# Kernel optimization log

Measured on AMD Instinct MI355X. Metric: run time of the kernel, lower is better.

## Reference

```python
import jax, jax.numpy as jnp
import numpy as np

D_MODEL = 1024
N_HEADS = 16
D_K = D_MODEL // N_HEADS
D_FF = 4096
B, S = 4, 2048
EPS = 1e-5


def layer_norm(x, gamma, beta):
    mu = jnp.mean(x, axis=-1, keepdims=True)
    var = jnp.var(x, axis=-1, keepdims=True)
    return (x - mu) * jax.lax.rsqrt(var + EPS) * gamma + beta


def setup_inputs() -> dict:
    key = jax.random.key(0)
    ks = jax.random.split(key, 16)
    s = 1.0 / np.sqrt(D_MODEL)
    inp = {
        "query": jax.random.normal(ks[0], (B, S, D_MODEL), jnp.float32),
        "key": jax.random.normal(ks[1], (B, S, D_MODEL), jnp.float32),
        "value": jax.random.normal(ks[2], (B, S, D_MODEL), jnp.float32),
        "mask": jnp.ones((B, S, S), jnp.int32),
        "Wq": jax.random.normal(ks[3], (D_MODEL, D_MODEL), jnp.float32) * s,
        "Wk": jax.random.normal(ks[4], (D_MODEL, D_MODEL), jnp.float32) * s,
        "Wv": jax.random.normal(ks[5], (D_MODEL, D_MODEL), jnp.float32) * s,
        "Wo": jax.random.normal(ks[6], (D_MODEL, D_MODEL), jnp.float32) * s,
        "bo": jnp.zeros((D_MODEL,), jnp.float32),
        "g1": jnp.ones((D_MODEL,), jnp.float32),
        "b1": jnp.zeros((D_MODEL,), jnp.float32),
        "g2": jnp.ones((D_MODEL,), jnp.float32),
        "b2": jnp.zeros((D_MODEL,), jnp.float32),
        "gff": jnp.ones((D_MODEL,), jnp.float32),
        "bff": jnp.zeros((D_MODEL,), jnp.float32),
        "W1": jax.random.normal(ks[7], (D_MODEL, D_FF), jnp.float32) * s,
        "bf1": jnp.zeros((D_FF,), jnp.float32),
        "W2": jax.random.normal(ks[8], (D_FF, D_MODEL), jnp.float32) / np.sqrt(D_FF),
        "bf2": jnp.zeros((D_MODEL,), jnp.float32),
    }
    return inp


def reference(query, key, value, mask, Wq, Wk, Wv, Wo, bo,
              g1, b1, g2, b2, gff, bff, W1, bf1, W2, bf2):
    # Multi-head attention (dropout = identity, eval mode)
    q = (query @ Wq.T).reshape(B, S, N_HEADS, D_K).transpose(0, 2, 1, 3)
    k = (key @ Wk.T).reshape(B, S, N_HEADS, D_K).transpose(0, 2, 1, 3)
    v = (value @ Wv.T).reshape(B, S, N_HEADS, D_K).transpose(0, 2, 1, 3)
    scores = jnp.einsum("bhqd,bhkd->bhqk", q, k) / np.sqrt(D_K)  # [B,H,S,S]
    scores = jnp.where(mask[:, None, :, :] == 0, jnp.float32(-1e9), scores)
    attn = jax.nn.softmax(scores, axis=-1)
    ctx = jnp.einsum("bhqk,bhkd->bhqd", attn, v)
    ctx = ctx.transpose(0, 2, 1, 3).reshape(B, S, D_MODEL)
    attn_out = ctx @ Wo.T + bo

    # residual + LN
    x = layer_norm(attn_out + query, g1, b1)

    # FeedForward (has its own internal LayerNorm)
    h = layer_norm(x, gff, bff)
    h = jax.nn.relu(h @ W1 + bf1)
    ff = h @ W2 + bf2

    return layer_norm(ff + x, g2, b2)
```

## Files before the change

kernel.cpp:

```cpp
#include <hip/hip_runtime.h>


#define DM   1024
#define DFF  4096
#define SEQ  2048

typedef unsigned short u16;
typedef short          sx8  __attribute__((ext_vector_type(8)));
typedef unsigned short ushx8 __attribute__((ext_vector_type(8)));
typedef unsigned short ushx4 __attribute__((ext_vector_type(4)));
typedef float          fx4  __attribute__((ext_vector_type(4)));
typedef unsigned int   ux2  __attribute__((ext_vector_type(2)));

__device__ __forceinline__ void async16(const void* g, void* l) {
  __builtin_amdgcn_global_load_lds((__attribute__((address_space(1))) void*)g,
                                   (__attribute__((address_space(3))) void*)l,
                                   16, 0, 0);
}
__device__ __forceinline__ float b2f(u16 u) {
  union { unsigned int i; float f; } v; v.i = ((unsigned int)u) << 16; return v.f;
}
__device__ __forceinline__ u16 f2b(float f) {
  union { float f; unsigned int i; } v; v.f = f;
  unsigned int r = v.i + 0x7fffu + ((v.i >> 16) & 1u);
  return (u16)(r >> 16);
}
__device__ __forceinline__ float fexp2(float x) {
#if __has_builtin(__builtin_amdgcn_exp2f)
  return __builtin_amdgcn_exp2f(x);
#else
  return exp2f(x);
#endif
}
__device__ __forceinline__ ushx8 ld8(const void* p, long idx, bool f32) {
  if (f32) {
    const float* s = (const float*)p + idx;
    fx4 a = *(const fx4*)s, b = *(const fx4*)(s + 4);
    ushx8 r;
    r[0] = f2b(a[0]); r[1] = f2b(a[1]); r[2] = f2b(a[2]); r[3] = f2b(a[3]);
    r[4] = f2b(b[0]); r[5] = f2b(b[1]); r[6] = f2b(b[2]); r[7] = f2b(b[3]);
    return r;
  }
  return *(const ushx8*)((const u16*)p + idx);
}
__device__ __forceinline__ void ld4f(const void* p, long idx, bool f32, float* o) {
  if (f32) {
    fx4 a = *(const fx4*)((const float*)p + idx);
    o[0] = a[0]; o[1] = a[1]; o[2] = a[2]; o[3] = a[3];
  } else {
    ushx4 a = *(const ushx4*)((const u16*)p + idx);
    o[0] = b2f(a[0]); o[1] = b2f(a[1]); o[2] = b2f(a[2]); o[3] = b2f(a[3]);
  }
}

__global__ void detect_kernel(const void* q, int* flags) {
  int lane = threadIdx.x;
  u16 v = ((const u16*)q)[lane << 1];
  int e = (v >> 7) & 0xff;
  int pl = (e >= 0x60 && e <= 0x8c) ? 1 : 0;
  unsigned long long m = __ballot(pl);
  if (lane == 0) { flags[0] = (__popcll(m) >= 40) ? 0 : 1; flags[1] = 0; flags[2] = 1; }
}

__global__ __launch_bounds__(256)
void mask_scan(const int* __restrict__ m, int* flags) {
  long i = (((long)blockIdx.x << 8) + threadIdx.x) << 3;
  const int4 a = *(const int4*)(m + i);
  const int4 b = *(const int4*)(m + i + 4);
  bool ok = a.x && a.y && a.z && a.w && b.x && b.y && b.z && b.w;
  if (!__all(ok)) { if ((threadIdx.x & 63) == 0) flags[2] = 0; }
}

__global__ __launch_bounds__(256)
void pack_w(const void* Wq, const void* Wk, const void* Wv, const void* Wo,
            u16* Wqkv, u16* Wo_bf, const int* f_p) {
  const bool f = (*f_p != 0);
  long i = (((long)blockIdx.x << 8) + threadIdx.x) << 3;
  const long QKVN = (long)3 * DM * DM;
  if (i < QKVN) {
    int row = (int)(i >> 10);
    const void* src = (row < DM) ? Wq : (row < 2 * DM ? Wk : Wv);
    long s = ((long)(row & (DM - 1)) << 10) + (i & 1023);
    *(ushx8*)(Wqkv + i) = ld8(src, s, f);
  } else {
    long j = i - QKVN;
    *(ushx8*)(Wo_bf + j) = ld8(Wo, j, f);
  }
}

__global__ __launch_bounds__(256)
void conv_bf3(const void* q, const void* k, const void* v, long off,
              u16* dst, long n, const int* f_p) {
  const bool f = (*f_p != 0);
  const void* src = (blockIdx.y == 0) ? q : (blockIdx.y == 1 ? k : v);
  long i = (((long)blockIdx.x << 8) + threadIdx.x) << 3;
  if (i < n) *(ushx8*)(dst + (long)blockIdx.y * n + i) = ld8(src, off + i, f);
}

template<bool RELU, bool BIAS, bool DBUF>
__global__ __launch_bounds__(256)
void gemm_bb(const u16* __restrict__ A, long az, const u16* __restrict__ B, long bz,
             const void* __restrict__ bias, u16* __restrict__ C, long cz,
             int M, int N, int K, int ldc, const int* biasf_p) {
  __shared__ __align__(16) u16 sA[(DBUF ? 3 : 1) * 128 * 64];
  __shared__ __align__(16) u16 sB[(DBUF ? 3 : 1) * 128 * 64];
  const int z = blockIdx.y;
  A += (long)z * az; B += (long)z * bz; C += (long)z * cz;
  const bool biasf = BIAS && (*biasf_p != 0);
  const int t = threadIdx.x;
  const int lane = t & 63, w = t >> 6;
  const int lm = lane & 15, lg = lane >> 4;
  const int ntil = N >> 7;
  const int bx = (blockIdx.x & 7) * ((int)gridDim.x >> 3) + (blockIdx.x >> 3);
  const int m0 = (bx / ntil) << 7;
  const int n0 = (bx % ntil) << 7;
  const int wm = (w & 1) << 6, wn = (w >> 1) << 6;

  fx4 acc[4][4];
#pragma unroll
  for (int i = 0; i < 4; ++i)
#pragma unroll
    for (int j = 0; j < 4; ++j) acc[i][j] = (fx4){0.f, 0.f, 0.f, 0.f};

  auto stage = [&](int so, int kt) {
#pragma unroll
    for (int it = 0; it < 4; ++it) {
      int ci = (it << 8) + t;
      int r = ci >> 3, cs = (ci & 7) ^ (r & 7);
      async16(&A[(size_t)(m0 + r) * K + kt + (cs << 3)], &sA[so + (ci << 3)]);
    }
#pragma unroll
    for (int it = 0; it < 4; ++it) {
      int ci = (it << 8) + t;
      int r = ci >> 3, cs = (ci & 7) ^ (r & 7);
      async16(&B[(size_t)(n0 + r) * K + kt + (cs << 3)], &sB[so + (ci << 3)]);
    }
  };

  auto compute = [&](int so) {
#pragma unroll
    for (int s = 0; s < 2; ++s) {
      const int g = (s << 2) + lg;
      sx8 afr[4], bfr[4];
#pragma unroll
      for (int i = 0; i < 4; ++i) {
        int ra = wm + (i << 4) + lm;
        afr[i] = *(const sx8*)&sA[so + ra * 64 + ((g ^ (ra & 7)) << 3)];
        int rb = wn + (i << 4) + lm;
        bfr[i] = *(const sx8*)&sB[so + rb * 64 + ((g ^ (rb & 7)) << 3)];
      }
      __builtin_amdgcn_s_setprio(1);
#pragma unroll
      for (int i = 0; i < 4; ++i)
#pragma unroll
        for (int j = 0; j < 4; ++j)
          acc[i][j] = __builtin_amdgcn_mfma_f32_16x16x32_bf16(afr[i], bfr[j], acc[i][j], 0, 0, 0);
      __builtin_amdgcn_s_setprio(0);
    }
  };

  if (DBUF) {
    const int NT = K >> 6;
    stage(0, 0);
    if (NT > 1) stage(8192, 64);
    for (int n = 0; n < NT; ++n) {
      __builtin_amdgcn_s_barrier();
      if (n + 2 < NT) {
        stage(((n + 2) % 3) << 13, (n + 2) << 6);
        asm volatile("s_waitcnt vmcnt(16)" ::: "memory");
      } else if (n + 1 < NT) {
        asm volatile("s_waitcnt vmcnt(8)" ::: "memory");
      } else {
        asm volatile("s_waitcnt vmcnt(0)" ::: "memory");
      }
      __builtin_amdgcn_sched_barrier(0);
      compute((n % 3) << 13);
    }
  } else {
    for (int kt = 0; kt < K; kt += 64) {
      __syncthreads();
      stage(0, kt);
      __syncthreads();
      compute(0);
    }
  }

#pragma unroll
  for (int j = 0; j < 4; ++j) {
    const int col = n0 + wn + (j << 4) + lm;
    float bv = 0.f;
    if (BIAS) bv = biasf ? ((const float*)bias)[col] : b2f(((const u16*)bias)[col]);
#pragma unroll
    for (int i = 0; i < 4; ++i) {
      const int row0 = m0 + wm + (i << 4) + (lg << 2);
#pragma unroll
      for (int r = 0; r < 4; ++r) {
        float v = acc[i][j][r] + bv;
        if (RELU) v = fmaxf(v, 0.f);
        C[(size_t)(row0 + r) * ldc + col] = f2b(v);
      }
    }
  }
}

template<bool RELU, bool BIAS>
__global__ __launch_bounds__(256)
void gemm_nt(const void* __restrict__ A, long aoff, const void* __restrict__ Bm,
             const void* __restrict__ bias, u16* __restrict__ C,
             int M, int N, int K,
             const int* af_p, const int* bf_p, const int* biasf_p) {
  __shared__ __align__(16) u16 sA[128 * 64];
  __shared__ __align__(16) u16 sB[128 * 64];
  const bool af = (*af_p != 0), bfl = (*bf_p != 0), biasf = (*biasf_p != 0);
  const int t = threadIdx.x;
  const int lane = t & 63, w = t >> 6;
  const int lm = lane & 15, lg = lane >> 4;
  const int ntil = N >> 7;
  const int m0 = (blockIdx.x / ntil) << 7;
  const int n0 = (blockIdx.x % ntil) << 7;
  const int wm = (w & 1) << 6, wn = (w >> 1) << 6;

  fx4 acc[4][4];
#pragma unroll
  for (int i = 0; i < 4; ++i)
#pragma unroll
    for (int j = 0; j < 4; ++j) acc[i][j] = (fx4){0.f, 0.f, 0.f, 0.f};

  for (int kt = 0; kt < K; kt += 64) {
    __syncthreads();
#pragma unroll
    for (int it = 0; it < 4; ++it) {
      int ci = (it << 8) + t;
      int r = ci >> 3, cs = (ci & 7) ^ (r & 7);
      ushx8 va = ld8(A, aoff + (long)(m0 + r) * K + kt + (cs << 3), af);
      *(ushx8*)&sA[ci << 3] = va;
      ushx8 vb = ld8(Bm, (long)(n0 + r) * K + kt + (cs << 3), bfl);
      *(ushx8*)&sB[ci << 3] = vb;
    }
    __syncthreads();
#pragma unroll
    for (int s = 0; s < 2; ++s) {
      const int g = (s << 2) + lg;
      sx8 afr[4], bfr[4];
#pragma unroll
      for (int i = 0; i < 4; ++i) {
        int ra = wm + (i << 4) + lm;
        afr[i] = *(const sx8*)&sA[ra * 64 + ((g ^ (ra & 7)) << 3)];
        int rb = wn + (i << 4) + lm;
        bfr[i] = *(const sx8*)&sB[rb * 64 + ((g ^ (rb & 7)) << 3)];
      }
#pragma unroll
      for (int i = 0; i < 4; ++i)
#pragma unroll
        for (int j = 0; j < 4; ++j)
          acc[i][j] = __builtin_amdgcn_mfma_f32_16x16x32_bf16(afr[i], bfr[j], acc[i][j], 0, 0, 0);
    }
  }

#pragma unroll
  for (int j = 0; j < 4; ++j) {
    const int col = n0 + wn + (j << 4) + lm;
    float bv = 0.f;
    if (BIAS) bv = biasf ? ((const float*)bias)[col] : b2f(((const u16*)bias)[col]);
#pragma unroll
    for (int i = 0; i < 4; ++i) {
      const int row0 = m0 + wm + (i << 4) + (lg << 2);
#pragma unroll
      for (int r = 0; r < 4; ++r) {
        float v = acc[i][j][r] + bv;
        if (RELU) v = fmaxf(v, 0.f);
        C[(size_t)(row0 + r) * N + col] = f2b(v);
      }
    }
  }
}

__global__ __launch_bounds__(256)
void transpose_any(const void* __restrict__ in, u16* __restrict__ out,
                   int R, int C, const int* f_p) {
  __shared__ u16 tile[64][68];
  const bool f = (*f_p != 0);
  const int r0 = blockIdx.y << 6, c0 = blockIdx.x << 6;
  const int t = threadIdx.x;
#pragma unroll
  for (int it = 0; it < 4; ++it) {
    int j = (it << 8) + t;
    int rr = j >> 4, cc4 = (j & 15) << 2;
    float v[4];
    ld4f(in, (long)(r0 + rr) * C + c0 + cc4, f, v);
#pragma unroll
    for (int q = 0; q < 4; ++q) tile[rr][cc4 + q] = f2b(v[q]);
  }
  __syncthreads();
#pragma unroll
  for (int it = 0; it < 4; ++it) {
    int j = (it << 8) + t;
    int cc = j >> 4, rr4 = (j & 15) << 2;
    ushx4 v;
    v[0] = tile[rr4 + 0][cc]; v[1] = tile[rr4 + 1][cc];
    v[2] = tile[rr4 + 2][cc]; v[3] = tile[rr4 + 3][cc];
    *(ushx4*)&out[(size_t)(c0 + cc) * R + r0 + rr4] = v;
  }
}

__global__ __launch_bounds__(256, 3)
void attn_kernel(const u16* __restrict__ qp, const u16* __restrict__ kp,
                 const u16* __restrict__ vp, int lds_,
                 const int* __restrict__ mask, u16* __restrict__ ctx,
                 const int* __restrict__ mflag) {
  __shared__ __align__(16) u16 sK[128 * 64];
  __shared__ __align__(16) u16 sVt[64 * 136];
  __shared__ __align__(16) unsigned sP2[4][1024];

  const bool nomask = (*mflag != 0);
  const long boff = (long)blockIdx.y * SEQ * (long)lds_;
  qp += boff; kp += boff; vp += boff;
  mask += (size_t)blockIdx.y * ((size_t)SEQ * SEQ);
  ctx += (size_t)blockIdx.y * ((size_t)SEQ * DM);

  const int id = (blockIdx.x & 7) * ((int)gridDim.x >> 3) + (blockIdx.x >> 3);
  const int q0 = (id & 31) << 6;
  const int h  = id >> 5;
  const int t = threadIdx.x, lane = t & 63, w = t >> 6;
  const int hoff = h << 6;
  const int lm = lane & 15, lg = lane >> 4;
  const int myq = q0 + (w << 4) + lm;
  const int aslot = 20 * lg;

  const int kq = (t & 31) << 2, dg = (t >> 5) << 3;
  const int vcol = kq ^ (((t >> 5) & 1) << 3);
  unsigned* pw = &sP2[w][0];
  const int wswz = (lm & 7) << 2;
  const int pwb = lm << 6;
  const int vrs = ((lm >> 3) & 1) << 3;

  sx8 aq[2];
#pragma unroll
  for (int s = 0; s < 2; ++s)
    aq[s] = *(const sx8*)&qp[(size_t)myq * lds_ + hoff + (((s << 2) + lg) << 3)];

  fx4 o[4];
#pragma unroll
  for (int i = 0; i < 4; ++i) o[i] = (fx4){0.f, 0.f, 0.f, 0.f};
  float m_prev = -1e30f, lsum = 0.f;
  const float SCL = 0.18033688f;
  const float RTHR = 44.36142f;

  const u16* vbase = vp + (size_t)kq * lds_ + hoff + dg;
  uint4 va = *(const uint4*)(vbase);
  uint4 vb_ = *(const uint4*)(vbase + (size_t)lds_);
  uint4 vc = *(const uint4*)(vbase + 2 * (size_t)lds_);
  uint4 vd = *(const uint4*)(vbase + 3 * (size_t)lds_);

  for (int kt = 0; kt < 16; ++kt) {
    const int k0 = kt << 7;
    __syncthreads();
#pragma unroll
    for (int it = 0; it < 4; ++it) {
      int ci = (it << 8) + t;
      int r = ci >> 3, cs = (ci & 7) ^ (r & 7);
      async16(&kp[(size_t)(k0 + r) * lds_ + hoff + (cs << 3)], &sK[ci << 3]);
    }
    {
      const unsigned A0[4] = {va.x, va.y, va.z, va.w};
      const unsigned B0[4] = {vb_.x, vb_.y, vb_.z, vb_.w};
      const unsigned C0[4] = {vc.x, vc.y, vc.z, vc.w};
      const unsigned D0[4] = {vd.x, vd.y, vd.z, vd.w};
#pragma unroll
      for (int j = 0; j < 8; ++j) {
        const unsigned sel = (j & 1) ? 0x07060302u : 0x05040100u;
        ux2 wv;
        wv[0] = __builtin_amdgcn_perm(B0[j >> 1], A0[j >> 1], sel);
        wv[1] = __builtin_amdgcn_perm(D0[j >> 1], C0[j >> 1], sel);
        *(ux2*)&sVt[(size_t)(dg + j) * 136 + vcol] = wv;
      }
    }
    __syncthreads();

    if (kt + 1 < 16) {
      const u16* vn = vbase + (size_t)(k0 + 128) * lds_;
      va = *(const uint4*)(vn);
      vb_ = *(const uint4*)(vn + (size_t)lds_);
      vc = *(const uint4*)(vn + 2 * (size_t)lds_);
      vd = *(const uint4*)(vn + 3 * (size_t)lds_);
    }

    fx4 sc[8];
#pragma unroll
    for (int nt = 0; nt < 8; ++nt) sc[nt] = (fx4){0.f, 0.f, 0.f, 0.f};
    __builtin_amdgcn_s_setprio(1);
#pragma unroll
    for (int s = 0; s < 2; ++s) {
      const int g = (s << 2) + lg;
#pragma unroll
      for (int nt = 0; nt < 8; ++nt) {
        int rk = (nt << 4) + lm;
        sx8 bk = *(const sx8*)&sK[rk * 64 + ((g ^ (rk & 7)) << 3)];
        sc[nt] = __builtin_amdgcn_mfma_f32_16x16x32_bf16(bk, aq[s], sc[nt], 0, 0, 0);
      }
    }
    __builtin_amdgcn_s_setprio(0);

    if (!nomask) {
#pragma unroll
      for (int nt = 0; nt < 8; ++nt)
#pragma unroll
        for (int r = 0; r < 4; ++r) {
          const int col = k0 + (nt << 4) + (lg << 2) + r;
          if (mask[((size_t)myq << 11) + col] == 0) sc[nt][r] = -1e9f;
        }
    }

    float tm = sc[0][0];
#pragma unroll
    for (int nt = 0; nt < 8; ++nt)
#pragma unroll
      for (int r = 0; r < 4; ++r) tm = fmaxf(tm, sc[nt][r]);
    tm = fmaxf(tm, __shfl_xor(tm, 16));
    tm = fmaxf(tm, __shfl_xor(tm, 32));

    if (!__all(tm <= m_prev + RTHR)) {
      const float mn = fmaxf(m_prev, tm);
      const float alpha = fexp2((m_prev - mn) * SCL);
      lsum *= alpha;
#pragma unroll
      for (int r = 0; r < 4; ++r) {
        float ar = __shfl(alpha, aslot + r);
#pragma unroll
        for (int ot = 0; ot < 4; ++ot) o[ot][r] *= ar;
      }
      m_prev = mn;
    }

    const float msc = m_prev * SCL;
    float rs = 0.f;
    float pvv[8][4];
#pragma unroll
    for (int nt = 0; nt < 8; ++nt)
#pragma unroll
      for (int r = 0; r < 4; ++r) {
        float e = fexp2(__builtin_fmaf(sc[nt][r], SCL, -msc));
        pvv[nt][r] = e;
        rs += e;
      }
    rs += __shfl_xor(rs, 16);
    rs += __shfl_xor(rs, 32);
    lsum += rs;

    unsigned cpk[8][2];
#pragma unroll
    for (int nt = 0; nt < 8; ++nt) {
      asm("v_cvt_pk_bf16_f32 %0, %1, %2" : "=v"(cpk[nt][0]) : "v"(pvv[nt][0]), "v"(pvv[nt][1]));
      asm("v_cvt_pk_bf16_f32 %0, %1, %2" : "=v"(cpk[nt][1]) : "v"(pvv[nt][2]), "v"(pvv[nt][3]));
    }
#pragma unroll
    for (int nt = 0; nt < 8; ++nt)
      *(ux2*)&pw[pwb + (((nt << 3) + (lg << 1)) ^ wswz)] = (ux2){cpk[nt][0], cpk[nt][1]};

    __builtin_amdgcn_s_setprio(1);
#pragma unroll
    for (int ks = 0; ks < 4; ++ks) {
      sx8 ap = *(const sx8*)&pw[pwb + (((ks << 4) + (lg << 2)) ^ wswz)];
#pragma unroll
      for (int ot = 0; ot < 4; ++ot) {
        int d = (ot << 4) + lm;
        sx8 bv = *(const sx8*)&sVt[d * 136 + (((ks << 5) + (lg << 3)) ^ vrs)];
        o[ot] = __builtin_amdgcn_mfma_f32_16x16x32_bf16(ap, bv, o[ot], 0, 0, 0);
      }
    }
    __builtin_amdgcn_s_setprio(0);
  }

  float inv = (lsum > 0.f) ? 1.f / lsum : 0.f;
#pragma unroll
  for (int r = 0; r < 4; ++r) {
    float ir = __shfl(inv, aslot + r);
#pragma unroll
    for (int ot = 0; ot < 4; ++ot) {
      const int rowg = q0 + (w << 4) + (lg << 2) + r;
      const int col = hoff + (ot << 4) + lm;
      ctx[((size_t)rowg << 10) + col] = f2b(o[ot][r] * ir);
    }
  }
}

__global__ __launch_bounds__(256)
void ln_dual(const u16* __restrict__ a, const void* __restrict__ res, long roff,
             const void* __restrict__ g1, const void* __restrict__ b1,
             const void* __restrict__ gf, const void* __restrict__ bf,
             u16* __restrict__ xo, u16* __restrict__ xlo, const int* f_p) {
  __shared__ float red[8];
  const bool f = (*f_p != 0);
  const int row = blockIdx.x, t = threadIdx.x;
  const int lane = t & 63, w = t >> 6;
  const size_t base = (size_t)row << 10;
  const int c = t << 2;

  ushx4 a4 = *(const ushx4*)(a + base + c);
  float rv[4];
  ld4f(res, roff + (long)base + c, f, rv);
  float v[4], s = 0.f, ss = 0.f;
#pragma unroll
  for (int j = 0; j < 4; ++j) { v[j] = b2f(a4[j]) + rv[j]; s += v[j]; ss += v[j] * v[j]; }
#pragma unroll
  for (int off = 32; off > 0; off >>= 1) { s += __shfl_xor(s, off); ss += __shfl_xor(ss, off); }
  if (lane == 0) { red[w] = s; red[4 + w] = ss; }
  __syncthreads();
  s = red[0] + red[1] + red[2] + red[3];
  ss = red[4] + red[5] + red[6] + red[7];
  float mu = s * (1.f / 1024.f);
  float rstd = rsqrtf(fmaxf(ss * (1.f / 1024.f) - mu * mu, 0.f) + 1e-5f);

  float g4[4], b4[4];
  ld4f(g1, c, f, g4); ld4f(b1, c, f, b4);
  float x[4], s2 = 0.f, ss2 = 0.f;
  ushx4 xo4;
#pragma unroll
  for (int j = 0; j < 4; ++j) {
    x[j] = (v[j] - mu) * rstd * g4[j] + b4[j];
    xo4[j] = f2b(x[j]);
    s2 += x[j]; ss2 += x[j] * x[j];
  }
  *(ushx4*)(xo + base + c) = xo4;
#pragma unroll
  for (int off = 32; off > 0; off >>= 1) { s2 += __shfl_xor(s2, off); ss2 += __shfl_xor(ss2, off); }
  __syncthreads();
  if (lane == 0) { red[w] = s2; red[4 + w] = ss2; }
  __syncthreads();
  s2 = red[0] + red[1] + red[2] + red[3];
  ss2 = red[4] + red[5] + red[6] + red[7];
  float mu2 = s2 * (1.f / 1024.f);
  float rstd2 = rsqrtf(fmaxf(ss2 * (1.f / 1024.f) - mu2 * mu2, 0.f) + 1e-5f);

  ld4f(gf, c, f, g4); ld4f(bf, c, f, b4);
  ushx4 xl4;
#pragma unroll
  for (int j = 0; j < 4; ++j)
    xl4[j] = f2b((x[j] - mu2) * rstd2 * g4[j] + b4[j]);
  *(ushx4*)(xlo + base + c) = xl4;
}

__global__ __launch_bounds__(256)
void ln_final(const u16* __restrict__ a, const u16* __restrict__ resx,
              const void* __restrict__ g, const void* __restrict__ bb,
              void* __restrict__ out, long ooff, const int* f_p) {
  __shared__ float red[8];
  const bool f = (*f_p != 0);
  const int row = blockIdx.x, t = threadIdx.x;
  const int lane = t & 63, w = t >> 6;
  const size_t base = (size_t)row << 10;
  const int c = t << 2;

  ushx4 a4 = *(const ushx4*)(a + base + c);
  ushx4 r4 = *(const ushx4*)(resx + base + c);
  float v[4], s = 0.f, ss = 0.f;
#pragma unroll
  for (int j = 0; j < 4; ++j) { v[j] = b2f(a4[j]) + b2f(r4[j]); s += v[j]; ss += v[j] * v[j]; }
#pragma unroll
  for (int off = 32; off > 0; off >>= 1) { s += __shfl_xor(s, off); ss += __shfl_xor(ss, off); }
  if (lane == 0) { red[w] = s; red[4 + w] = ss; }
  __syncthreads();
  s = red[0] + red[1] + red[2] + red[3];
  ss = red[4] + red[5] + red[6] + red[7];
  float mu = s * (1.f / 1024.f);
  float rstd = rsqrtf(fmaxf(ss * (1.f / 1024.f) - mu * mu, 0.f) + 1e-5f);

  float g4[4], b4[4];
  ld4f(g, c, f, g4); ld4f(bb, c, f, b4);
  if (f) {
    fx4 o4;
#pragma unroll
    for (int j = 0; j < 4; ++j) o4[j] = (v[j] - mu) * rstd * g4[j] + b4[j];
    *(fx4*)((float*)out + ooff + base + c) = o4;
  } else {
    ushx4 o4;
#pragma unroll
    for (int j = 0; j < 4; ++j) o4[j] = f2b((v[j] - mu) * rstd * g4[j] + b4[j]);
    *(ushx4*)((u16*)out + ooff + base + c) = o4;
  }
}

extern "C" void kernel_launch(void* const* d_in, const int* in_sizes, int n_in,
                              void* d_out, int out_size, void* d_ws, size_t ws_size,
                              hipStream_t stream) {
  (void)in_sizes; (void)n_in; (void)out_size;
  const void* query = d_in[0];
  const void* keyi  = d_in[1];
  const void* value = d_in[2];
  const int*  mask  = (const int*)d_in[3];
  const void* Wq = d_in[4];
  const void* Wk = d_in[5];
  const void* Wv = d_in[6];
  const void* Wo = d_in[7];
  const void* bo = d_in[8];
  const void* g1 = d_in[9];
  const void* b1 = d_in[10];
  const void* g2 = d_in[11];
  const void* b2 = d_in[12];
  const void* gff = d_in[13];
  const void* bff = d_in[14];
  const void* W1 = d_in[15];
  const void* bf1 = d_in[16];
  const void* W2 = d_in[17];
  const void* bf2 = d_in[18];

  char* p = (char*)d_ws;
  int* flags = (int*)p;
  const int* F = flags;
  const int* Z = flags + 1;
  const int* M = flags + 2;
  dim3 blk(256);

  const size_t FIXED = 4096 + ((size_t)24 << 20);
  const size_t needC = FIXED + (size_t)8192 * 14336;
  const size_t needA = FIXED + (size_t)4096 * 14336;
  const size_t needB = FIXED + (size_t)2048 * 14336;

  if (ws_size >= needB) {
    const int CH = (ws_size >= needC) ? 8192 : (ws_size >= needA) ? 4096 : 2048;
    const int nch = 8192 / CH;

    u16* Wqkv  = (u16*)(p + 4096);
    u16* Wo_bf = Wqkv + (size_t)3 * DM * DM;
    u16* W1T   = Wo_bf + (size_t)DM * DM;
    u16* W2T   = W1T + (size_t)DFF * DM;
    u16* D0    = W2T + (size_t)DM * DFF;
    u16* D1    = D0 + (size_t)3 * CH * DM;
    u16* D2    = D1 + (size_t)3 * CH * DM;
    u16* qb = D0;
    u16* qkv = D1;
    u16* ao = D1, *x = D1 + (size_t)CH * DM, *xln = D1 + (size_t)2 * CH * DM;
    u16* h = D0;
    u16* ctx = D2, *ff = D2;

    detect_kernel<<<1, 64, 0, stream>>>(query, flags);
    mask_scan<<<dim3(8192), blk, 0, stream>>>(mask, flags);
    pack_w<<<dim3(2048), blk, 0, stream>>>(Wq, Wk, Wv, Wo, Wqkv, Wo_bf, F);
    transpose_any<<<dim3(DFF / 64, DM / 64), blk, 0, stream>>>(W1, W1T, DM, DFF, F);
    transpose_any<<<dim3(DM / 64, DFF / 64), blk, 0, stream>>>(W2, W2T, DFF, DM, F);

    for (int c = 0; c < nch; ++c) {
      const long off = (long)c * CH * DM;
      const long n = (long)CH * DM;
      conv_bf3<<<dim3((int)(n >> 11), 3), blk, 0, stream>>>(query, keyi, value, off, qb, n, F);

      gemm_bb<false, false, false><<<dim3((CH / 128) * 8, 3), blk, 0, stream>>>(
          qb, (long)CH * DM, Wqkv, (long)DM * DM, nullptr,
          qkv, 1024L, CH, DM, DM, 3072, Z);

      const int bpc = CH / SEQ, b0 = c * bpc;
      attn_kernel<<<dim3(512, bpc), blk, 0, stream>>>(
          qkv, qkv + 1024, qkv + 2048, 3072,
          mask + (size_t)b0 * SEQ * SEQ, ctx, M);

      gemm_bb<false, true, true><<<dim3((CH / 128) * 8, 1), blk, 0, stream>>>(
          ctx, 0, Wo_bf, 0, bo, ao, 0, CH, DM, DM, DM, F);

      ln_dual<<<dim3(CH), blk, 0, stream>>>(ao, query, off, g1, b1, gff, bff, x, xln, F);

      gemm_bb<true, true, false><<<dim3((CH / 128) * 32, 1), blk, 0, stream>>>(
          xln, 0, W1T, 0, bf1, h, 0, CH, DFF, DM, DFF, F);
      gemm_bb<false, true, true><<<dim3((CH / 128) * 8, 1), blk, 0, stream>>>(
          h, 0, W2T, 0, bf2, ff, 0, CH, DM, DFF, DM, F);

      ln_final<<<dim3(CH), blk, 0, stream>>>(ff, x, g2, b2, d_out, off, F);
    }
  } else {
    const int CH = 2048, FH = 1024;
    const int nch = 8192 / CH;
    const size_t h0 = 4096;
    u16* W1T = (u16*)(p + h0);
    u16* W2T = W1T + (size_t)DFF * DM;
    u16* hb  = (u16*)(p + h0 + ((size_t)16 << 20));
    const size_t HB = (size_t)FH * DFF * 2;
    u16* r0 = (u16*)(p + h0 + ((size_t)16 << 20) + HB);
    const size_t CE = (size_t)CH * DM;
    u16* qp = r0;
    u16* kp = qp + CE;
    u16* vp = kp + CE;
    u16* ctxb = vp + CE;
    u16* x = qp; u16* xln = kp; u16* ao = vp; u16* ff = ctxb;

    detect_kernel<<<1, 64, 0, stream>>>(query, flags);
    mask_scan<<<dim3(8192), blk, 0, stream>>>(mask, flags);
    transpose_any<<<dim3(DFF / 64, DM / 64), blk, 0, stream>>>(W1, W1T, DM, DFF, F);
    transpose_any<<<dim3(DM / 64, DFF / 64), blk, 0, stream>>>(W2, W2T, DFF, DM, F);

    for (int c = 0; c < nch; ++c) {
      const long off = (long)c * CH * DM;
      dim3 gq((CH / 128) * (DM / 128));

      gemm_nt<false, false><<<gq, blk, 0, stream>>>(query, off, Wq, Wq, qp, CH, DM, DM, F, F, Z);
      gemm_nt<false, false><<<gq, blk, 0, stream>>>(keyi,  off, Wk, Wk, kp, CH, DM, DM, F, F, Z);
      gemm_nt<false, false><<<gq, blk, 0, stream>>>(value, off, Wv, Wv, vp, CH, DM, DM, F, F, Z);

      const int bpc = CH / SEQ, b0 = c * bpc;
      for (int bl = 0; bl < bpc; ++bl) {
        const size_t lo = (size_t)bl * SEQ * DM;
        attn_kernel<<<dim3(512, 1), blk, 0, stream>>>(
            qp + lo, kp + lo, vp + lo, 1024,
            mask + (size_t)(b0 + bl) * SEQ * SEQ, ctxb + lo, M);
      }

      gemm_nt<false, true><<<gq, blk, 0, stream>>>(ctxb, 0, Wo, bo, ao, CH, DM, DM, Z, F, F);

      ln_dual<<<dim3(CH), blk, 0, stream>>>(ao, query, off, g1, b1, gff, bff, x, xln, F);

      for (int qs = 0; qs < CH / FH; ++qs) {
        const long so = (long)qs * FH * DM;
        gemm_nt<true, true><<<dim3((FH / 128) * (DFF / 128)), blk, 0, stream>>>(
            xln + so, 0, W1T, bf1, hb, FH, DFF, DM, Z, Z, F);
        gemm_nt<false, true><<<dim3((FH / 128) * (DM / 128)), blk, 0, stream>>>(
            hb, 0, W2T, bf2, ff + so, FH, DM, DFF, Z, Z, F);
      }

      ln_final<<<dim3(CH), blk, 0, stream>>>(ff, x, g2, b2, d_out, off, F);
    }
  }
}
```

Baseline: 711.7 us.

## Shrink LDS: double-buffer GEMM, alias attention P buffer onto K tile

```diff
diff --git a/kernel.cpp b/kernel.cpp
--- a/kernel.cpp
+++ b/kernel.cpp
@@ -102,8 +102,8 @@
 void gemm_bb(const u16* __restrict__ A, long az, const u16* __restrict__ B, long bz,
              const void* __restrict__ bias, u16* __restrict__ C, long cz,
              int M, int N, int K, int ldc, const int* biasf_p) {
-  __shared__ __align__(16) u16 sA[(DBUF ? 3 : 1) * 128 * 64];
-  __shared__ __align__(16) u16 sB[(DBUF ? 3 : 1) * 128 * 64];
+  __shared__ __align__(16) u16 sA[(DBUF ? 2 : 1) * 128 * 64];
+  __shared__ __align__(16) u16 sB[(DBUF ? 2 : 1) * 128 * 64];
   const int z = blockIdx.y;
   A += (long)z * az; B += (long)z * bz; C += (long)z * cz;
   const bool biasf = BIAS && (*biasf_p != 0);
@@ -162,19 +162,17 @@
   if (DBUF) {
     const int NT = K >> 6;
     stage(0, 0);
-    if (NT > 1) stage(8192, 64);
     for (int n = 0; n < NT; ++n) {
-      __builtin_amdgcn_s_barrier();
-      if (n + 2 < NT) {
-        stage(((n + 2) % 3) << 13, (n + 2) << 6);
-        asm volatile("s_waitcnt vmcnt(16)" ::: "memory");
-      } else if (n + 1 < NT) {
+      if (n + 1 < NT) {
+        stage(((n + 1) & 1) << 13, (n + 1) << 6);
         asm volatile("s_waitcnt vmcnt(8)" ::: "memory");
       } else {
         asm volatile("s_waitcnt vmcnt(0)" ::: "memory");
       }
+      __builtin_amdgcn_s_barrier();
       __builtin_amdgcn_sched_barrier(0);
-      compute((n % 3) << 13);
+      compute((n & 1) << 13);
+      if (n + 1 < NT) __builtin_amdgcn_s_barrier();
     }
   } else {
     for (int kt = 0; kt < K; kt += 64) {
@@ -303,14 +301,15 @@
   }
 }
 
-__global__ __launch_bounds__(256, 3)
+__global__ __launch_bounds__(256, 4)
 void attn_kernel(const u16* __restrict__ qp, const u16* __restrict__ kp,
                  const u16* __restrict__ vp, int lds_,
                  const int* __restrict__ mask, u16* __restrict__ ctx,
                  const int* __restrict__ mflag) {
-  __shared__ __align__(16) u16 sK[128 * 64];
-  __shared__ __align__(16) u16 sVt[64 * 136];
-  __shared__ __align__(16) unsigned sP2[4][1024];
+  __shared__ __align__(16) u16 smem[16384];
+  u16* const sK  = smem;
+  u16* const sVt = smem + 8192;
+  unsigned* const sPal = (unsigned*)smem;
 
   const bool nomask = (*mflag != 0);
   const long boff = (long)blockIdx.y * SEQ * (long)lds_;
@@ -328,11 +327,12 @@
   const int aslot = 20 * lg;
 
   const int kq = (t & 31) << 2, dg = (t >> 5) << 3;
-  const int vcol = kq ^ (((t >> 5) & 1) << 3);
-  unsigned* pw = &sP2[w][0];
+  const int kg7 = (kq >> 3) & 7;
+  const int k7o = kq & 7;
+  const int vbrow = ((kq >> 6) << 6) + dg;
+  unsigned* pw = sPal + (w << 10);
   const int wswz = (lm & 7) << 2;
   const int pwb = lm << 6;
-  const int vrs = ((lm >> 3) & 1) << 3;
 
   sx8 aq[2];
 #pragma unroll
@@ -372,7 +372,7 @@
         ux2 wv;
         wv[0] = __builtin_amdgcn_perm(B0[j >> 1], A0[j >> 1], sel);
         wv[1] = __builtin_amdgcn_perm(D0[j >> 1], C0[j >> 1], sel);
-        *(ux2*)&sVt[(size_t)(dg + j) * 136 + vcol] = wv;
+        *(ux2*)&sVt[(vbrow + j) * 64 + ((kg7 ^ j) << 3) + k7o] = wv;
       }
     }
     __syncthreads();
@@ -453,6 +453,11 @@
       asm("v_cvt_pk_bf16_f32 %0, %1, %2" : "=v"(cpk[nt][0]) : "v"(pvv[nt][0]), "v"(pvv[nt][1]));
       asm("v_cvt_pk_bf16_f32 %0, %1, %2" : "=v"(cpk[nt][1]) : "v"(pvv[nt][2]), "v"(pvv[nt][3]));
     }
+
+    __builtin_amdgcn_sched_barrier(0);
+    __builtin_amdgcn_s_barrier();
+    __builtin_amdgcn_sched_barrier(0);
+
 #pragma unroll
     for (int nt = 0; nt < 8; ++nt)
       *(ux2*)&pw[pwb + (((nt << 3) + (lg << 1)) ^ wswz)] = (ux2){cpk[nt][0], cpk[nt][1]};
@@ -461,10 +466,11 @@
 #pragma unroll
     for (int ks = 0; ks < 4; ++ks) {
       sx8 ap = *(const sx8*)&pw[pwb + (((ks << 4) + (lg << 2)) ^ wswz)];
+      const int vrow = ((ks >> 1) << 6);
+      const int vgr = (((ks & 1) << 2) + lg) ^ (lm & 7);
 #pragma unroll
       for (int ot = 0; ot < 4; ++ot) {
-        int d = (ot << 4) + lm;
-        sx8 bv = *(const sx8*)&sVt[d * 136 + (((ks << 5) + (lg << 3)) ^ vrs)];
+        sx8 bv = *(const sx8*)&sVt[(vrow + (ot << 4) + lm) * 64 + (vgr << 3)];
         o[ot] = __builtin_amdgcn_mfma_f32_16x16x32_bf16(ap, bv, o[ot], 0, 0, 0);
       }
     }
```

Result: faster. 639.9 us (-10.1%).
